# Kernel tuning notes

Hardware: AMD Instinct MI355X
Metric: run time of the kernel (lower is better)

## Reference

```python
import jax, jax.numpy as jnp
import numpy as np

NUM_HEADS = 16
ROPE_BASE = 10000.0


def _rotate_half(x):
    d = x.shape[-1] // 2
    return jnp.concatenate([-x[..., d:], x[..., :d]], axis=-1)


def _rope_cos_sin(seq_len, rot_dim, dtype):
    # LlamaRotaryEmbedding(dim=rot_dim): inv_freq over even indices, emb = cat(freqs, freqs)
    inv_freq = 1.0 / (ROPE_BASE ** (jnp.arange(0, rot_dim, 2, dtype=jnp.float32) / rot_dim))
    t = jnp.arange(seq_len, dtype=jnp.float32)
    freqs = t[:, None] * inv_freq[None, :]            # [S, rot_dim/2]
    emb = jnp.concatenate([freqs, freqs], axis=-1)    # [S, rot_dim]
    return jnp.cos(emb).astype(dtype), jnp.sin(emb).astype(dtype)


def setup_inputs() -> dict:
    key = jax.random.key(0)
    ks = jax.random.split(key, 9)
    B, S, H = 2, 2048, 2048
    L = H // 8
    s = 0.02
    return {
        "hidden_states": jax.random.normal(ks[0], (B, S, H), jnp.float32),
        "Wkv_d": jax.random.normal(ks[1], (H, L), jnp.float32) * s,
        "Wq_d": jax.random.normal(ks[2], (H, L), jnp.float32) * s,
        "Wk_u": jax.random.normal(ks[3], (L, H // 2), jnp.float32) * s,
        "Wq_u": jax.random.normal(ks[4], (L, H // 2), jnp.float32) * s,
        "Wv_u": jax.random.normal(ks[5], (L, H), jnp.float32) * s,
        "Wrk": jax.random.normal(ks[6], (H, H // 2), jnp.float32) * s,
        "Wrq": jax.random.normal(ks[7], (L, H // 2), jnp.float32) * s,
        "Wo": jax.random.normal(ks[8], (H, H), jnp.float32) * s,
    }


def reference(hidden_states, Wkv_d, Wq_d, Wk_u, Wq_u, Wv_u, Wrk, Wrq, Wo):
    B, S, H = hidden_states.shape
    nh = NUM_HEADS
    hd = H // nh          # 128
    rd = hd // 2          # 64 (rope / content half width)

    kv_d = hidden_states @ Wkv_d            # [B,S,L]
    q_d = hidden_states @ Wq_d              # [B,S,L]

    k_c = (kv_d @ Wk_u).reshape(B, S, nh, rd)
    q_c = (q_d @ Wq_u).reshape(B, S, nh, rd)
    v = (kv_d @ Wv_u).reshape(B, S, nh, hd)
    k_r = (hidden_states @ Wrk).reshape(B, S, nh, rd)
    q_r = (q_d @ Wrq).reshape(B, S, nh, rd)

    cos, sin = _rope_cos_sin(S, rd, hidden_states.dtype)
    cos = cos[None, :, None, :]             # [1,S,1,rd] broadcast over batch/heads
    sin = sin[None, :, None, :]
    q_r = q_r * cos + _rotate_half(q_r) * sin
    k_r = k_r * cos + _rotate_half(k_r) * sin

    q = jnp.concatenate([q_c, q_r], axis=-1).transpose(0, 2, 1, 3)  # [B,nh,S,hd]
    k = jnp.concatenate([k_c, k_r], axis=-1).transpose(0, 2, 1, 3)
    v = v.transpose(0, 2, 1, 3)

    scale = jnp.asarray(hd, q.dtype) ** -0.5
    scores = jnp.einsum("bhqd,bhkd->bhqk", q, k) * scale
    causal = jnp.tril(jnp.ones((S, S), dtype=bool))
    scores = jnp.where(causal[None, None], scores, jnp.finfo(scores.dtype).min)
    attn = jax.nn.softmax(scores, axis=-1)
    y = jnp.einsum("bhqk,bhkd->bhqd", attn, v)
    y = y.transpose(0, 2, 1, 3).reshape(B, S, H)
    return y @ Wo
```

## Files before the change

kernel.cpp:

```cpp
#include <hip/hip_runtime.h>
#include <hip/hip_bf16.h>
#include <math.h>


typedef __attribute__((ext_vector_type(8))) short bf16x8;
typedef __attribute__((ext_vector_type(4))) float f32x4;
typedef unsigned int u32;

#define MFMA16(a, b, c) __builtin_amdgcn_mfma_f32_16x16x32_bf16(a, b, c, 0, 0, 0)

__device__ __forceinline__ short f2bs(float f) {
  __hip_bfloat16 h = __float2bfloat16(f);
  return *reinterpret_cast<short*>(&h);
}
__device__ __forceinline__ float bs2f(short s) {
  union { unsigned int u; float f; } v;
  v.u = ((unsigned int)(unsigned short)s) << 16;
  return v.f;
}
__device__ __forceinline__ u32 fbits(float f) {
  union { float f; u32 u; } v; v.f = f; return v.u;
}

__device__ __forceinline__ void async16(const void* g, void* l) {
  __builtin_amdgcn_global_load_lds(
      (const __attribute__((address_space(1))) u32*)(unsigned long long)g,
      (__attribute__((address_space(3))) u32*)(unsigned int)(unsigned long long)l,
      16, 0, 0);
}
__device__ __forceinline__ void wait_vm0() {
  __builtin_amdgcn_s_waitcnt(0x0f70);
}

__device__ __forceinline__ void wtrans_tile(const float* __restrict__ W,
                                            short* __restrict__ Wt, int K, int N,
                                            int bx, int by, int tid) {
  __shared__ float t[32][33];
  int k0 = by * 32, n0 = bx * 32;
#pragma unroll
  for (int i = 0; i < 4; ++i) {
    int idx = tid + i * 256;
    int r = idx >> 5, c = idx & 31;
    t[r][c] = W[(size_t)(k0 + r) * N + n0 + c];
  }
  __syncthreads();
#pragma unroll
  for (int i = 0; i < 4; ++i) {
    int idx = tid + i * 256;
    int r = idx >> 5, c = idx & 31;
    Wt[(size_t)(n0 + r) * K + k0 + c] = f2bs(t[c][r]);
  }
}

__global__ __launch_bounds__(256) void prep_all(
    const float* __restrict__ hs, const float* __restrict__ Wkvd,
    const float* __restrict__ Wqd, const float* __restrict__ Wku,
    const float* __restrict__ Wqu, const float* __restrict__ Wvu,
    const float* __restrict__ Wrk, const float* __restrict__ Wrq,
    const float* __restrict__ Wo, short* __restrict__ hs_b,
    short* __restrict__ W1t, short* __restrict__ W2t,
    short* __restrict__ W3t, short* __restrict__ Wo_t) {
  const int b = blockIdx.x, tid = threadIdx.x;
  if (b < 8192) {
    int i = (b * 256 + tid) * 4;
    float4 v = *(const float4*)(hs + i);
    short4 o;
    o.x = f2bs(v.x); o.y = f2bs(v.y); o.z = f2bs(v.z); o.w = f2bs(v.w);
    *(short4*)(hs_b + i) = o;
  } else if (b < 8704) {
    int l = b - 8192; wtrans_tile(Wkvd, W1t, 2048, 256, l & 7, l >> 3, tid);
  } else if (b < 9216) {
    int l = b - 8704; wtrans_tile(Wqd, W1t + 256 * 2048, 2048, 256, l & 7, l >> 3, tid);
  } else if (b < 11264) {
    int l = b - 9216; wtrans_tile(Wrk, W1t + 512 * 2048, 2048, 1024, l & 31, l >> 5, tid);
  } else if (b < 11520) {
    int l = b - 11264; wtrans_tile(Wku, W2t, 256, 1024, l & 31, l >> 5, tid);
  } else if (b < 12032) {
    int l = b - 11520; wtrans_tile(Wvu, W2t + 1024 * 256, 256, 2048, l & 63, l >> 6, tid);
  } else if (b < 12288) {
    int l = b - 12032; wtrans_tile(Wqu, W3t, 256, 1024, l & 31, l >> 5, tid);
  } else if (b < 12544) {
    int l = b - 12288; wtrans_tile(Wrq, W3t + 1024 * 256, 256, 1024, l & 31, l >> 5, tid);
  } else {
    int l = b - 12544; wtrans_tile(Wo, Wo_t, 2048, 2048, l & 63, l >> 6, tid);
  }
}

__device__ __forceinline__ void cstore(float v, float* p) { *p = v; }
__device__ __forceinline__ void cstore(float v, short* p) { *p = f2bs(v); }

template <typename CT>
__global__ __launch_bounds__(256) void gemm_bt(const short* __restrict__ A, int lda,
                                               const short* __restrict__ Bt, int ldb,
                                               CT* __restrict__ C, int ldc, int K) {
  __shared__ short As[128 * 64];
  __shared__ short Bs[128 * 64];
  const int tid = threadIdx.x;
  const int wave = tid >> 6, lane = tid & 63;
  const int quad = lane >> 4, l15 = lane & 15;
  const int wm = wave & 1, wn = wave >> 1;
  const int row0 = blockIdx.y * 128, col0 = blockIdx.x * 128;
  const int sr = tid >> 3;
  const int sc = ((tid & 7) ^ (sr & 7)) * 8;
  const short* Ag = A + (size_t)(row0 + sr) * lda + sc;
  const short* Bg = Bt + (size_t)(col0 + sr) * ldb + sc;
  const int rk = l15 & 7;

  f32x4 acc[4][4];
#pragma unroll
  for (int i = 0; i < 4; ++i)
#pragma unroll
    for (int j = 0; j < 4; ++j) acc[i][j] = {0.f, 0.f, 0.f, 0.f};

  for (int k0 = 0; k0 < K; k0 += 64) {
    __syncthreads();
#pragma unroll
    for (int i = 0; i < 4; ++i) {
      async16(Ag + (size_t)(i * 32) * lda + k0, &As[i * 2048 + tid * 8]);
      async16(Bg + (size_t)(i * 32) * ldb + k0, &Bs[i * 2048 + tid * 8]);
    }
    wait_vm0();
    __syncthreads();
#pragma unroll
    for (int s = 0; s < 2; ++s) {
      bf16x8 af[4], bfr[4];
#pragma unroll
      for (int i = 0; i < 4; ++i) {
        af[i]  = *(const bf16x8*)&As[(wm * 64 + i * 16 + l15) * 64 +
                                     ((s * 4 + quad) ^ rk) * 8];
        bfr[i] = *(const bf16x8*)&Bs[(wn * 64 + i * 16 + l15) * 64 +
                                     ((s * 4 + quad) ^ rk) * 8];
      }
#pragma unroll
      for (int i = 0; i < 4; ++i)
#pragma unroll
        for (int j = 0; j < 4; ++j)
          acc[i][j] = MFMA16(af[i], bfr[j], acc[i][j]);
    }
  }
#pragma unroll
  for (int i = 0; i < 4; ++i)
#pragma unroll
    for (int j = 0; j < 4; ++j)
#pragma unroll
      for (int r = 0; r < 4; ++r) {
        int row = row0 + wm * 64 + i * 16 + quad * 4 + r;
        int col = col0 + wn * 64 + j * 16 + l15;
        cstore(acc[i][j][r], &C[(size_t)row * ldc + col]);
      }
}

__global__ __launch_bounds__(256) void gemm23(const short* __restrict__ C1,
                                              const short* __restrict__ W2t,
                                              short* __restrict__ C2,
                                              short* __restrict__ C3) {
  __shared__ short As[128 * 64];
  __shared__ short Bs[128 * 64];
  const int tid = threadIdx.x;
  const int wave = tid >> 6, lane = tid & 63;
  const int quad = lane >> 4, l15 = lane & 15;
  const int wm = wave & 1, wn = wave >> 1;
  const int bx = blockIdx.x;
  const bool isC2 = bx < 24;
  short* C = isC2 ? C2 : C3;
  const int ldc = isC2 ? 3072 : 2048;
  const int colbase = isC2 ? bx * 128 : (bx - 24) * 128;
  const short* A = isC2 ? C1 : C1 + 256;
  const int row0 = blockIdx.y * 128;
  const int sr = tid >> 3;
  const int sc = ((tid & 7) ^ (sr & 7)) * 8;
  const short* Ag = A + (size_t)(row0 + sr) * 1536 + sc;
  const short* Bg = W2t + (size_t)(bx * 128 + sr) * 256 + sc;
  const int rk = l15 & 7;

  f32x4 acc[4][4];
#pragma unroll
  for (int i = 0; i < 4; ++i)
#pragma unroll
    for (int j = 0; j < 4; ++j) acc[i][j] = {0.f, 0.f, 0.f, 0.f};

  for (int k0 = 0; k0 < 256; k0 += 64) {
    __syncthreads();
#pragma unroll
    for (int i = 0; i < 4; ++i) {
      async16(Ag + (size_t)(i * 32) * 1536 + k0, &As[i * 2048 + tid * 8]);
      async16(Bg + (size_t)(i * 32) * 256 + k0, &Bs[i * 2048 + tid * 8]);
    }
    wait_vm0();
    __syncthreads();
#pragma unroll
    for (int s = 0; s < 2; ++s) {
      bf16x8 af[4], bfr[4];
#pragma unroll
      for (int i = 0; i < 4; ++i) {
        af[i]  = *(const bf16x8*)&As[(wm * 64 + i * 16 + l15) * 64 +
                                     ((s * 4 + quad) ^ rk) * 8];
        bfr[i] = *(const bf16x8*)&Bs[(wn * 64 + i * 16 + l15) * 64 +
                                     ((s * 4 + quad) ^ rk) * 8];
      }
#pragma unroll
      for (int i = 0; i < 4; ++i)
#pragma unroll
        for (int j = 0; j < 4; ++j)
          acc[i][j] = MFMA16(af[i], bfr[j], acc[i][j]);
    }
  }
#pragma unroll
  for (int i = 0; i < 4; ++i)
#pragma unroll
    for (int j = 0; j < 4; ++j)
#pragma unroll
      for (int r = 0; r < 4; ++r) {
        int row = row0 + wm * 64 + i * 16 + quad * 4 + r;
        int col = colbase + wn * 64 + j * 16 + l15;
        cstore(acc[i][j][r], &C[(size_t)row * ldc + col]);
      }
}

__global__ __launch_bounds__(256) void rope_vtrans(
    const short* __restrict__ c3, const short* __restrict__ c2,
    const short* __restrict__ c1, short* __restrict__ qf,
    short* __restrict__ kf, short* __restrict__ vt) {
  if (blockIdx.x < 32768) {
    const float QSCALE = 0.08838834764831845f * 1.4426950408889634f;
    int idx = blockIdx.x * 256 + threadIdx.x;
    int m = idx >> 11;
    int col = idx & 2047;
    int h = col >> 7;
    int j = col & 127;
    int b = m >> 11, s = m & 2047;
    float oq, ok;
    if (j < 64) {
      oq = bs2f(c3[(size_t)m * 2048 + h * 64 + j]);
      ok = bs2f(c2[(size_t)m * 3072 + h * 64 + j]);
    } else {
      int jr = j - 64;
      int f = jr & 31;
      float ang = (float)s * __expf(-0.2878231366242557f * (float)f);
      float c = __cosf(ang), sn = __sinf(ang);
      size_t qb = (size_t)m * 2048 + 1024 + h * 64;
      size_t kb = (size_t)m * 1536 + 512 + h * 64;
      float xq = bs2f(c3[qb + jr]), xk = bs2f(c1[kb + jr]);
      float rq, rk;
      if (jr < 32) { rq = -bs2f(c3[qb + jr + 32]); rk = -bs2f(c1[kb + jr + 32]); }
      else         { rq =  bs2f(c3[qb + jr - 32]); rk =  bs2f(c1[kb + jr - 32]); }
      oq = fmaf(xq, c, rq * sn);
      ok = fmaf(xk, c, rk * sn);
    }
    size_t dst = (((size_t)b * 16 + h) * 2048 + s) * 128 + j;
    qf[dst] = f2bs(oq * QSCALE);
    kf[dst] = f2bs(ok);
  } else {
    __shared__ short t[64][72];
    const int l = blockIdx.x - 32768;
    const int bh = ((l & 7) << 2) | ((l >> 3) & 3);
    const int s0 = ((l >> 5) & 31) * 64;
    const int d0 = ((l >> 10) & 1) * 64;
    const int b = bh >> 4, h = bh & 15;
#pragma unroll
    for (int i = 0; i < 16; ++i) {
      int idx = threadIdx.x + i * 256;
      int r = idx >> 6, c = idx & 63;
      t[r][c] = c2[(size_t)(b * 2048 + s0 + r) * 3072 + 1024 + h * 128 + d0 + c];
    }
    __syncthreads();
#pragma unroll
    for (int i = 0; i < 16; ++i) {
      int idx = threadIdx.x + i * 256;
      int r = idx >> 6, c = idx & 63;
      vt[((size_t)bh * 128 + d0 + r) * 2048 + s0 + c] = t[c][r];
    }
  }
}

__global__ __launch_bounds__(256) void attn_split(const short* __restrict__ qf,
                                                  const short* __restrict__ kf,
                                                  const short* __restrict__ vt,
                                                  short* __restrict__ part,
                                                  float2* __restrict__ ml) {
  __shared__ short Ks[2][64 * 128];
  __shared__ short Vs[2][128 * 64];
  __shared__ short Pw[4][32 * 64];
  const int lid = blockIdx.x;
  const int bh = (lid & 7) * 4 + ((lid >> 3) & 3);
  const int x = lid >> 5;
  const int tid = threadIdx.x;
  const int wave = tid >> 6, lane = tid & 63;
  const int quad = lane >> 4, l15 = lane & 15;
  const int krow_l = tid >> 4;
  const int kcol_sw = ((tid & 15) ^ krow_l) * 8;
  const int vrow_l = tid >> 3;
  const int vcol_sw = ((tid & 7) ^ (vrow_l & 7)) * 8;
  const short* kgB = kf + (((size_t)bh * 2048) + krow_l) * 128 + kcol_sw;
  const short* vgB = vt + ((size_t)bh * 128 + vrow_l) * 2048 + vcol_sw;
  const int pswz = l15 & 14;

  for (int pass = 0; pass < 2; ++pass) {
    const int qt = pass == 0 ? x : 15 - x;
    const int ks = pass == 0 ? 0 : qt + 1;
    const int ke = (qt + 1) << pass;
    const int q0w = qt * 128 + wave * 32;

    bf16x8 qfr[2][4];
#pragma unroll
    for (int mi = 0; mi < 2; ++mi) {
      const short* qp = qf + (((size_t)bh * 2048) + q0w + mi * 16 + l15) * 128;
#pragma unroll
      for (int kc = 0; kc < 4; ++kc)
        qfr[mi][kc] = *(const bf16x8*)(qp + kc * 32 + quad * 8);
    }
    float m_i[2] = {-INFINITY, -INFINITY};
    float l_i[2] = {0.f, 0.f};
    f32x4 O[2][8];
#pragma unroll
    for (int mi = 0; mi < 2; ++mi)
#pragma unroll
      for (int dt = 0; dt < 8; ++dt) O[mi][dt] = {0.f, 0.f, 0.f, 0.f};

    {
      const short* kg = kgB + (size_t)ks * 64 * 128;
      const short* vg = vgB + ks * 64;
#pragma unroll
      for (int i = 0; i < 4; ++i) {
        async16(kg + (size_t)i * 16 * 128, &Ks[0][i * 2048 + tid * 8]);
        async16(vg + (size_t)i * 32 * 2048, &Vs[0][i * 2048 + tid * 8]);
      }
    }
    wait_vm0();
    __syncthreads();

    int cur = 0;
    for (int kt = ks; kt < ke; ++kt) {
      const int k0 = kt * 64;
      if (kt + 1 < ke) {
        const short* kg = kgB + (size_t)(k0 + 64) * 128;
        const short* vg = vgB + (k0 + 64);
#pragma unroll
        for (int i = 0; i < 4; ++i) {
          async16(kg + (size_t)i * 16 * 128, &Ks[cur ^ 1][i * 2048 + tid * 8]);
          async16(vg + (size_t)i * 32 * 2048, &Vs[cur ^ 1][i * 2048 + tid * 8]);
        }
      }

      f32x4 St[2][4];
#pragma unroll
      for (int mi = 0; mi < 2; ++mi)
#pragma unroll
        for (int j = 0; j < 4; ++j) St[mi][j] = {0.f, 0.f, 0.f, 0.f};
      __builtin_amdgcn_s_setprio(1);
#pragma unroll
      for (int kc = 0; kc < 4; ++kc) {
        bf16x8 kb[4];
#pragma unroll
        for (int j = 0; j < 4; ++j)
          kb[j] = *(const bf16x8*)&Ks[cur][(j * 16 + l15) * 128 +
                                          (((kc * 4 + quad) ^ l15) & 15) * 8];
#pragma unroll
        for (int mi = 0; mi < 2; ++mi)
#pragma unroll
          for (int j = 0; j < 4; ++j)
            St[mi][j] = MFMA16(kb[j], qfr[mi][kc], St[mi][j]);
      }
      __builtin_amdgcn_s_setprio(0);

      if (kt >= 2 * qt) {
#pragma unroll
        for (int mi = 0; mi < 2; ++mi)
#pragma unroll
          for (int j = 0; j < 4; ++j)
#pragma unroll
            for (int r = 0; r < 4; ++r)
              if (k0 + j * 16 + quad * 4 + r > q0w + mi * 16 + l15)
                St[mi][j][r] = -INFINITY;
      }

#pragma unroll
      for (int mi = 0; mi < 2; ++mi) {
        float mt = -INFINITY;
#pragma unroll
        for (int j = 0; j < 4; ++j)
#pragma unroll
          for (int r = 0; r < 4; ++r) mt = fmaxf(mt, St[mi][j][r]);
        if (!__all(mt <= m_i[mi] + 8.f)) {
          mt = fmaxf(mt, __shfl_xor(mt, 16));
          mt = fmaxf(mt, __shfl_xor(mt, 32));
          float mnew = fmaxf(m_i[mi], mt);
          float a = __builtin_amdgcn_exp2f(m_i[mi] - mnew);
          m_i[mi] = mnew;
          l_i[mi] *= a;
#pragma unroll
          for (int dt = 0; dt < 8; ++dt)
#pragma unroll
            for (int r = 0; r < 4; ++r) O[mi][dt][r] *= a;
        }
        float ms = (m_i[mi] == -INFINITY) ? 0.f : m_i[mi];
        float ps = 0.f;
#pragma unroll
        for (int j = 0; j < 4; ++j)
#pragma unroll
          for (int r = 0; r < 4; ++r) {
            float p = __builtin_amdgcn_exp2f(St[mi][j][r] - ms);
            St[mi][j][r] = p;
            ps += p;
          }
        l_i[mi] += ps;
      }

#pragma unroll
      for (int mi = 0; mi < 2; ++mi) {
        int pr = mi * 16 + l15;
#pragma unroll
        for (int j = 0; j < 4; ++j) {
          u32 u0 = (fbits(St[mi][j][1]) & 0xffff0000u) | (fbits(St[mi][j][0]) >> 16);
          u32 u1 = (fbits(St[mi][j][3]) & 0xffff0000u) | (fbits(St[mi][j][2]) >> 16);
          uint2 pk; pk.x = u0; pk.y = u1;
          int c8s = (j * 4 + quad) ^ pswz;
          *(uint2*)&Pw[wave][pr * 64 + c8s * 4] = pk;
        }
      }

      __builtin_amdgcn_s_setprio(1);
#pragma unroll
      for (int kc2 = 0; kc2 < 2; ++kc2) {
        bf16x8 pa[2];
#pragma unroll
        for (int mi = 0; mi < 2; ++mi) {
          int pr = mi * 16 + l15;
          int c8s = (kc2 * 8 + quad * 2) ^ pswz;
          pa[mi] = *(const bf16x8*)&Pw[wave][pr * 64 + c8s * 4];
        }
#pragma unroll
        for (int dt = 0; dt < 8; ++dt) {
          bf16x8 vb = *(const bf16x8*)&Vs[cur][(dt * 16 + l15) * 64 +
                                              (((kc2 * 4 + quad) ^ (l15 & 7)) & 7) * 8];
#pragma unroll
          for (int mi = 0; mi < 2; ++mi)
            O[mi][dt] = MFMA16(vb, pa[mi], O[mi][dt]);
        }
      }
      __builtin_amdgcn_s_setprio(0);

      wait_vm0();
      __syncthreads();
      cur ^= 1;
    }

    const int pidx = (bh * 16 + qt) * 2 + pass;
    short* pb = part + (size_t)pidx * 128 * 128;
#pragma unroll
    for (int mi = 0; mi < 2; ++mi) {
      int qrow = wave * 32 + mi * 16 + l15;
#pragma unroll
      for (int dt = 0; dt < 8; ++dt) {
        short4 o;
        o.x = f2bs(O[mi][dt][0]); o.y = f2bs(O[mi][dt][1]);
        o.z = f2bs(O[mi][dt][2]); o.w = f2bs(O[mi][dt][3]);
        *(short4*)&pb[(size_t)qrow * 128 + dt * 16 + quad * 4] = o;
      }
    }
    float lr[2];
#pragma unroll
    for (int mi = 0; mi < 2; ++mi) {
      float v = l_i[mi];
      v += __shfl_xor(v, 16);
      v += __shfl_xor(v, 32);
      lr[mi] = v;
    }
    if (quad == 0) {
#pragma unroll
      for (int mi = 0; mi < 2; ++mi) {
        float2 v; v.x = m_i[mi]; v.y = lr[mi];
        ml[pidx * 128 + wave * 32 + mi * 16 + l15] = v;
      }
    }
  }
}

__global__ __launch_bounds__(256) void attn_merge(const short* __restrict__ part,
                                                  const float2* __restrict__ ml,
                                                  short* __restrict__ y) {
  const int l = blockIdx.x;
  const int bh = ((l & 7) << 2) | ((l >> 3) & 3);
  const int qt = (l >> 5) & 15;
  const int b = bh >> 4, h = bh & 15;
  const int row = threadIdx.x >> 1, d0 = (threadIdx.x & 1) * 64;
  const int p1 = (bh * 16 + qt) * 2, p2 = p1 + 1;
  float2 a = ml[p1 * 128 + row], c = ml[p2 * 128 + row];
  float m = fmaxf(a.x, c.x);
  float a1 = __builtin_amdgcn_exp2f(a.x - m);
  float a2 = __builtin_amdgcn_exp2f(c.x - m);
  float invl = 1.f / (a.y * a1 + c.y * a2);
  a1 *= invl; a2 *= invl;
  const short* s1 = part + ((size_t)p1 * 128 + row) * 128 + d0;
  const short* s2 = part + ((size_t)p2 * 128 + row) * 128 + d0;
  short* yp = y + (((size_t)b * 2048 + qt * 128 + row) * 16 + h) * 128 + d0;
#pragma unroll
  for (int j = 0; j < 16; ++j) {
    short4 v1 = *(const short4*)(s1 + j * 4);
    short4 v2 = *(const short4*)(s2 + j * 4);
    short4 o;
    o.x = f2bs(bs2f(v1.x) * a1 + bs2f(v2.x) * a2);
    o.y = f2bs(bs2f(v1.y) * a1 + bs2f(v2.y) * a2);
    o.z = f2bs(bs2f(v1.z) * a1 + bs2f(v2.z) * a2);
    o.w = f2bs(bs2f(v1.w) * a1 + bs2f(v2.w) * a2);
    *(short4*)(yp + j * 4) = o;
  }
}

extern "C" void kernel_launch(void* const* d_in, const int* in_sizes, int n_in,
                              void* d_out, int out_size, void* d_ws, size_t ws_size,
                              hipStream_t stream) {
  const float* hs   = (const float*)d_in[0];
  const float* Wkvd = (const float*)d_in[1];
  const float* Wqd  = (const float*)d_in[2];
  const float* Wku  = (const float*)d_in[3];
  const float* Wqu  = (const float*)d_in[4];
  const float* Wvu  = (const float*)d_in[5];
  const float* Wrk  = (const float*)d_in[6];
  const float* Wrq  = (const float*)d_in[7];
  const float* Wo   = (const float*)d_in[8];
  float* out = (float*)d_out;
  char* ws = (char*)d_ws;
  const size_t MB = 1024ull * 1024ull;

  short* hs_b = (short*)(ws + 0 * MB);
  short* W1t  = (short*)(ws + 16 * MB);
  short* W2t  = (short*)(ws + 22 * MB);
  short* W3t  = W2t + 3072 * 256;
  short* C1   = (short*)(ws + 25 * MB);
  short* C2   = (short*)(ws + 37 * MB);
  short* C3   = (short*)(ws + 61 * MB);
  short* Wo_t = (short*)(ws + 77 * MB);
  short* q_f  = (short*)(ws + 85 * MB);
  short* k_f  = (short*)(ws + 101 * MB);
  short* v_t  = (short*)(ws + 117 * MB);
  short* y_b  = (short*)(ws + 133 * MB);
  short*  partb = (short*)(ws + 0 * MB);
  float2* mlb   = (float2*)(ws + 32 * MB);

  dim3 blk(256);
  prep_all<<<dim3(16640), blk, 0, stream>>>(hs, Wkvd, Wqd, Wku, Wqu, Wvu, Wrk,
                                            Wrq, Wo, hs_b, W1t, W2t, W3t, Wo_t);

  gemm_bt<short><<<dim3(12, 32), blk, 0, stream>>>(hs_b, 2048, W1t, 2048, C1, 1536, 2048);
  gemm23<<<dim3(40, 32), blk, 0, stream>>>(C1, W2t, C2, C3);

  rope_vtrans<<<dim3(34816), blk, 0, stream>>>(C3, C2, C1, q_f, k_f, v_t);

  attn_split<<<dim3(512), blk, 0, stream>>>(q_f, k_f, v_t, partb, mlb);
  attn_merge<<<dim3(512), blk, 0, stream>>>(partb, mlb, y_b);

  gemm_bt<float><<<dim3(16, 32), blk, 0, stream>>>(y_b, 2048, Wo_t, 2048, out, 2048, 2048);
}
```

Before: 351.4 us.

## Halve attention tile sizes to double block count in split attention

Shrinks the attention query tile from 128 to 64 rows (16 per wave) and the key tile from 64 to 32, doubling the grid of the split and merge kernels to 1024 blocks. Shared-memory swizzles, partial-output layout and merge indexing are rewritten for the smaller tiles. The aim is more parallelism and occupancy on a 256-CU device and less shared memory per block, at the cost of lower MFMA reuse per K/V load, more loop iterations and more barriers.

```diff
diff --git a/kernel.cpp b/kernel.cpp
--- a/kernel.cpp
+++ b/kernel.cpp
@@ -278,52 +278,49 @@
                                                   const short* __restrict__ vt,
                                                   short* __restrict__ part,
                                                   float2* __restrict__ ml) {
-  __shared__ short Ks[2][64 * 128];
-  __shared__ short Vs[2][128 * 64];
-  __shared__ short Pw[4][32 * 64];
+  __shared__ short Ks[2][32 * 128];
+  __shared__ short Vs[2][128 * 32];
+  __shared__ short Pw[4][16 * 32];
   const int lid = blockIdx.x;
   const int bh = (lid & 7) * 4 + ((lid >> 3) & 3);
-  const int x = lid >> 5;
+  const int x  = lid >> 5;
   const int tid = threadIdx.x;
   const int wave = tid >> 6, lane = tid & 63;
   const int quad = lane >> 4, l15 = lane & 15;
   const int krow_l = tid >> 4;
   const int kcol_sw = ((tid & 15) ^ krow_l) * 8;
-  const int vrow_l = tid >> 3;
-  const int vcol_sw = ((tid & 7) ^ (vrow_l & 7)) * 8;
+  const int vrow_l = tid >> 2;
+  const int vcol_sw = ((tid & 3) ^ (vrow_l & 3) ^ ((vrow_l >> 2) & 3)) * 8;
   const short* kgB = kf + (((size_t)bh * 2048) + krow_l) * 128 + kcol_sw;
   const short* vgB = vt + ((size_t)bh * 128 + vrow_l) * 2048 + vcol_sw;
-  const int pswz = l15 & 14;
+  const int pswz = l15 & 6;
 
   for (int pass = 0; pass < 2; ++pass) {
-    const int qt = pass == 0 ? x : 15 - x;
-    const int ks = pass == 0 ? 0 : qt + 1;
-    const int ke = (qt + 1) << pass;
-    const int q0w = qt * 128 + wave * 32;
-
-    bf16x8 qfr[2][4];
-#pragma unroll
-    for (int mi = 0; mi < 2; ++mi) {
-      const short* qp = qf + (((size_t)bh * 2048) + q0w + mi * 16 + l15) * 128;
+    const int qt = pass ? 31 - x : x;
+    const int ks = pass ? qt + 1 : 0;
+    const int ke = pass ? 2 * (qt + 1) : x + 1;
+    const int q0w = qt * 64 + wave * 16;
+
+    bf16x8 qfr[4];
+    {
+      const short* qp = qf + (((size_t)bh * 2048) + q0w + l15) * 128;
 #pragma unroll
       for (int kc = 0; kc < 4; ++kc)
-        qfr[mi][kc] = *(const bf16x8*)(qp + kc * 32 + quad * 8);
-    }
-    float m_i[2] = {-INFINITY, -INFINITY};
-    float l_i[2] = {0.f, 0.f};
-    f32x4 O[2][8];
-#pragma unroll
-    for (int mi = 0; mi < 2; ++mi)
-#pragma unroll
-      for (int dt = 0; dt < 8; ++dt) O[mi][dt] = {0.f, 0.f, 0.f, 0.f};
+        qfr[kc] = *(const bf16x8*)(qp + kc * 32 + quad * 8);
+    }
+    float m_i = -INFINITY;
+    float l_i = 0.f;
+    f32x4 O[8];
+#pragma unroll
+    for (int dt = 0; dt < 8; ++dt) O[dt] = {0.f, 0.f, 0.f, 0.f};
 
     {
-      const short* kg = kgB + (size_t)ks * 64 * 128;
-      const short* vg = vgB + ks * 64;
-#pragma unroll
-      for (int i = 0; i < 4; ++i) {
+      const short* kg = kgB + (size_t)ks * 32 * 128;
+      const short* vg = vgB + ks * 32;
+#pragma unroll
+      for (int i = 0; i < 2; ++i) {
         async16(kg + (size_t)i * 16 * 128, &Ks[0][i * 2048 + tid * 8]);
-        async16(vg + (size_t)i * 32 * 2048, &Vs[0][i * 2048 + tid * 8]);
+        async16(vg + (size_t)i * 64 * 2048, &Vs[0][i * 2048 + tid * 8]);
       }
     }
     wait_vm0();
@@ -331,112 +328,97 @@
 
     int cur = 0;
     for (int kt = ks; kt < ke; ++kt) {
-      const int k0 = kt * 64;
+      const int k0 = kt * 32;
       if (kt + 1 < ke) {
-        const short* kg = kgB + (size_t)(k0 + 64) * 128;
-        const short* vg = vgB + (k0 + 64);
-#pragma unroll
-        for (int i = 0; i < 4; ++i) {
+        const short* kg = kgB + (size_t)(kt + 1) * 32 * 128;
+        const short* vg = vgB + (kt + 1) * 32;
+#pragma unroll
+        for (int i = 0; i < 2; ++i) {
           async16(kg + (size_t)i * 16 * 128, &Ks[cur ^ 1][i * 2048 + tid * 8]);
-          async16(vg + (size_t)i * 32 * 2048, &Vs[cur ^ 1][i * 2048 + tid * 8]);
+          async16(vg + (size_t)i * 64 * 2048, &Vs[cur ^ 1][i * 2048 + tid * 8]);
         }
       }
 
-      f32x4 St[2][4];
-#pragma unroll
-      for (int mi = 0; mi < 2; ++mi)
-#pragma unroll
-        for (int j = 0; j < 4; ++j) St[mi][j] = {0.f, 0.f, 0.f, 0.f};
+      f32x4 St[2];
+#pragma unroll
+      for (int j = 0; j < 2; ++j) St[j] = {0.f, 0.f, 0.f, 0.f};
       __builtin_amdgcn_s_setprio(1);
 #pragma unroll
       for (int kc = 0; kc < 4; ++kc) {
-        bf16x8 kb[4];
-#pragma unroll
-        for (int j = 0; j < 4; ++j)
+        bf16x8 kb[2];
+#pragma unroll
+        for (int j = 0; j < 2; ++j)
           kb[j] = *(const bf16x8*)&Ks[cur][(j * 16 + l15) * 128 +
                                           (((kc * 4 + quad) ^ l15) & 15) * 8];
 #pragma unroll
-        for (int mi = 0; mi < 2; ++mi)
-#pragma unroll
-          for (int j = 0; j < 4; ++j)
-            St[mi][j] = MFMA16(kb[j], qfr[mi][kc], St[mi][j]);
+        for (int j = 0; j < 2; ++j)
+          St[j] = MFMA16(kb[j], qfr[kc], St[j]);
       }
       __builtin_amdgcn_s_setprio(0);
 
       if (kt >= 2 * qt) {
 #pragma unroll
-        for (int mi = 0; mi < 2; ++mi)
-#pragma unroll
-          for (int j = 0; j < 4; ++j)
-#pragma unroll
-            for (int r = 0; r < 4; ++r)
-              if (k0 + j * 16 + quad * 4 + r > q0w + mi * 16 + l15)
-                St[mi][j][r] = -INFINITY;
-      }
-
-#pragma unroll
-      for (int mi = 0; mi < 2; ++mi) {
+        for (int j = 0; j < 2; ++j)
+#pragma unroll
+          for (int r = 0; r < 4; ++r)
+            if (k0 + j * 16 + quad * 4 + r > q0w + l15)
+              St[j][r] = -INFINITY;
+      }
+
+      {
         float mt = -INFINITY;
 #pragma unroll
-        for (int j = 0; j < 4; ++j)
-#pragma unroll
-          for (int r = 0; r < 4; ++r) mt = fmaxf(mt, St[mi][j][r]);
-        if (!__all(mt <= m_i[mi] + 8.f)) {
+        for (int j = 0; j < 2; ++j)
+#pragma unroll
+          for (int r = 0; r < 4; ++r) mt = fmaxf(mt, St[j][r]);
+        if (!__all(mt <= m_i + 8.f)) {
           mt = fmaxf(mt, __shfl_xor(mt, 16));
           mt = fmaxf(mt, __shfl_xor(mt, 32));
-          float mnew = fmaxf(m_i[mi], mt);
-          float a = __builtin_amdgcn_exp2f(m_i[mi] - mnew);
-          m_i[mi] = mnew;
-          l_i[mi] *= a;
+          float mnew = fmaxf(m_i, mt);
+          float a = __builtin_amdgcn_exp2f(m_i - mnew);
+          m_i = mnew;
+          l_i *= a;
 #pragma unroll
           for (int dt = 0; dt < 8; ++dt)
 #pragma unroll
-            for (int r = 0; r < 4; ++r) O[mi][dt][r] *= a;
+            for (int r = 0; r < 4; ++r) O[dt][r] *= a;
         }
-        float ms = (m_i[mi] == -INFINITY) ? 0.f : m_i[mi];
+        float ms = (m_i == -INFINITY) ? 0.f : m_i;
         float ps = 0.f;
 #pragma unroll
-        for (int j = 0; j < 4; ++j)
+        for (int j = 0; j < 2; ++j)
 #pragma unroll
           for (int r = 0; r < 4; ++r) {
-            float p = __builtin_amdgcn_exp2f(St[mi][j][r] - ms);
-            St[mi][j][r] = p;
+            float p = __builtin_amdgcn_exp2f(St[j][r] - ms);
+            St[j][r] = p;
             ps += p;
           }
-        l_i[mi] += ps;
-      }
-
-#pragma unroll
-      for (int mi = 0; mi < 2; ++mi) {
-        int pr = mi * 16 + l15;
-#pragma unroll
-        for (int j = 0; j < 4; ++j) {
-          u32 u0 = (fbits(St[mi][j][1]) & 0xffff0000u) | (fbits(St[mi][j][0]) >> 16);
-          u32 u1 = (fbits(St[mi][j][3]) & 0xffff0000u) | (fbits(St[mi][j][2]) >> 16);
+        l_i += ps;
+      }
+
+      {
+        int pr = l15;
+#pragma unroll
+        for (int j = 0; j < 2; ++j) {
+          u32 u0 = (fbits(St[j][1]) & 0xffff0000u) | (fbits(St[j][0]) >> 16);
+          u32 u1 = (fbits(St[j][3]) & 0xffff0000u) | (fbits(St[j][2]) >> 16);
           uint2 pk; pk.x = u0; pk.y = u1;
-          int c8s = (j * 4 + quad) ^ pswz;
-          *(uint2*)&Pw[wave][pr * 64 + c8s * 4] = pk;
+          int g = (j * 4 + quad) ^ pswz;
+          *(uint2*)&Pw[wave][pr * 32 + g * 4] = pk;
         }
       }
 
       __builtin_amdgcn_s_setprio(1);
-#pragma unroll
-      for (int kc2 = 0; kc2 < 2; ++kc2) {
-        bf16x8 pa[2];
-#pragma unroll
-        for (int mi = 0; mi < 2; ++mi) {
-          int pr = mi * 16 + l15;
-          int c8s = (kc2 * 8 + quad * 2) ^ pswz;
-          pa[mi] = *(const bf16x8*)&Pw[wave][pr * 64 + c8s * 4];
-        }
-#pragma unroll
-        for (int dt = 0; dt < 8; ++dt) {
-          bf16x8 vb = *(const bf16x8*)&Vs[cur][(dt * 16 + l15) * 64 +
-                                              (((kc2 * 4 + quad) ^ (l15 & 7)) & 7) * 8];
-#pragma unroll
-          for (int mi = 0; mi < 2; ++mi)
-            O[mi][dt] = MFMA16(vb, pa[mi], O[mi][dt]);
-        }
+      bf16x8 pa;
+      {
+        int g = (quad * 2) ^ pswz;
+        pa = *(const bf16x8*)&Pw[wave][l15 * 32 + g * 4];
+      }
+#pragma unroll
+      for (int dt = 0; dt < 8; ++dt) {
+        bf16x8 vb = *(const bf16x8*)&Vs[cur][(dt * 16 + l15) * 32 +
+                                            ((quad ^ (l15 & 3) ^ ((l15 >> 2) & 3)) & 3) * 8];
+        O[dt] = MFMA16(vb, pa, O[dt]);
       }
       __builtin_amdgcn_s_setprio(0);
 
@@ -445,33 +427,24 @@
       cur ^= 1;
     }
 
-    const int pidx = (bh * 16 + qt) * 2 + pass;
-    short* pb = part + (size_t)pidx * 128 * 128;
-#pragma unroll
-    for (int mi = 0; mi < 2; ++mi) {
-      int qrow = wave * 32 + mi * 16 + l15;
+    const int pidx = (bh * 32 + qt) * 2 + pass;
+    short* pb = part + (size_t)pidx * 64 * 128;
+    {
+      int qrow = wave * 16 + l15;
 #pragma unroll
       for (int dt = 0; dt < 8; ++dt) {
         short4 o;
-        o.x = f2bs(O[mi][dt][0]); o.y = f2bs(O[mi][dt][1]);
-        o.z = f2bs(O[mi][dt][2]); o.w = f2bs(O[mi][dt][3]);
+        o.x = f2bs(O[dt][0]); o.y = f2bs(O[dt][1]);
+        o.z = f2bs(O[dt][2]); o.w = f2bs(O[dt][3]);
         *(short4*)&pb[(size_t)qrow * 128 + dt * 16 + quad * 4] = o;
       }
     }
-    float lr[2];
-#pragma unroll
-    for (int mi = 0; mi < 2; ++mi) {
-      float v = l_i[mi];
-      v += __shfl_xor(v, 16);
-      v += __shfl_xor(v, 32);
-      lr[mi] = v;
-    }
+    float lr = l_i;
+    lr += __shfl_xor(lr, 16);
+    lr += __shfl_xor(lr, 32);
     if (quad == 0) {
-#pragma unroll
-      for (int mi = 0; mi < 2; ++mi) {
-        float2 v; v.x = m_i[mi]; v.y = lr[mi];
-        ml[pidx * 128 + wave * 32 + mi * 16 + l15] = v;
-      }
+      float2 v; v.x = m_i; v.y = lr;
+      ml[pidx * 64 + wave * 16 + l15] = v;
     }
   }
 }
@@ -481,21 +454,21 @@
                                                   short* __restrict__ y) {
   const int l = blockIdx.x;
   const int bh = ((l & 7) << 2) | ((l >> 3) & 3);
-  const int qt = (l >> 5) & 15;
+  const int qt = (l >> 5) & 31;
   const int b = bh >> 4, h = bh & 15;
-  const int row = threadIdx.x >> 1, d0 = (threadIdx.x & 1) * 64;
-  const int p1 = (bh * 16 + qt) * 2, p2 = p1 + 1;
-  float2 a = ml[p1 * 128 + row], c = ml[p2 * 128 + row];
+  const int row = threadIdx.x >> 2, d0 = (threadIdx.x & 3) * 32;
+  const int p1 = (bh * 32 + qt) * 2, p2 = p1 + 1;
+  float2 a = ml[p1 * 64 + row], c = ml[p2 * 64 + row];
   float m = fmaxf(a.x, c.x);
   float a1 = __builtin_amdgcn_exp2f(a.x - m);
   float a2 = __builtin_amdgcn_exp2f(c.x - m);
   float invl = 1.f / (a.y * a1 + c.y * a2);
   a1 *= invl; a2 *= invl;
-  const short* s1 = part + ((size_t)p1 * 128 + row) * 128 + d0;
-  const short* s2 = part + ((size_t)p2 * 128 + row) * 128 + d0;
-  short* yp = y + (((size_t)b * 2048 + qt * 128 + row) * 16 + h) * 128 + d0;
-#pragma unroll
-  for (int j = 0; j < 16; ++j) {
+  const short* s1 = part + ((size_t)p1 * 64 + row) * 128 + d0;
+  const short* s2 = part + ((size_t)p2 * 64 + row) * 128 + d0;
+  short* yp = y + (((size_t)b * 2048 + qt * 64 + row) * 16 + h) * 128 + d0;
+#pragma unroll
+  for (int j = 0; j < 8; ++j) {
     short4 v1 = *(const short4*)(s1 + j * 4);
     short4 v2 = *(const short4*)(s2 + j * 4);
     short4 o;
@@ -547,8 +520,8 @@
 
   rope_vtrans<<<dim3(34816), blk, 0, stream>>>(C3, C2, C1, q_f, k_f, v_t);
 
-  attn_split<<<dim3(512), blk, 0, stream>>>(q_f, k_f, v_t, partb, mlb);
-  attn_merge<<<dim3(512), blk, 0, stream>>>(partb, mlb, y_b);
+  attn_split<<<dim3(1024), blk, 0, stream>>>(q_f, k_f, v_t, partb, mlb);
+  attn_merge<<<dim3(1024), blk, 0, stream>>>(partb, mlb, y_b);
 
   gemm_bt<float><<<dim3(16, 32), blk, 0, stream>>>(y_b, 2048, Wo_t, 2048, out, 2048, 2048);
 }
```

Measured after the change: 331.0 us. -5.8%, faster.
